# Kernel optimization log

Hardware: AMD Instinct MI355X
Metric: run time of the kernel (lower is better)

Reference implementation:

```python
import jax, jax.numpy as jnp
import numpy as np

B, S, HID = 1, 2048, 4096
N_HEADS, N_KV, HEAD_DIM = 32, 8, 128
N_REP = N_HEADS // N_KV
ROPE_THETA = 10000.0
NEG_INF = -1e9


def setup_inputs() -> dict:
    key = jax.random.key(0)
    ks = jax.random.split(key, 5)
    hidden_states = jax.random.normal(ks[0], (B, S, HID), dtype=jnp.float32)
    Wq = jax.random.normal(ks[1], (HID, N_HEADS * HEAD_DIM), dtype=jnp.float32) * 0.02
    Wk = jax.random.normal(ks[2], (HID, N_KV * HEAD_DIM), dtype=jnp.float32) * 0.02
    Wv = jax.random.normal(ks[3], (HID, N_KV * HEAD_DIM), dtype=jnp.float32) * 0.02
    Wo = jax.random.normal(ks[4], (N_HEADS * HEAD_DIM, HID), dtype=jnp.float32) * 0.02
    # causal additive mask [B, 1, S, S]
    causal = jnp.tril(jnp.ones((S, S), dtype=bool))
    attention_mask = jnp.where(causal, 0.0, NEG_INF).astype(jnp.float32)[None, None]
    position_ids = jnp.broadcast_to(jnp.arange(S, dtype=jnp.int32)[None], (B, S))
    return {
        "hidden_states": hidden_states, "Wq": Wq, "Wk": Wk, "Wv": Wv, "Wo": Wo,
        "attention_mask": attention_mask, "position_ids": position_ids,
    }


def _rotate_half(x):
    half = x.shape[-1] // 2
    return jnp.concatenate([-x[..., half:], x[..., :half]], axis=-1)


def _rope_tables(position_ids):
    # inv_freq: [head_dim/2]
    inv_freq = 1.0 / (ROPE_THETA ** (jnp.arange(0, HEAD_DIM, 2, dtype=jnp.float32) / HEAD_DIM))
    # freqs: [B, S, head_dim/2]
    freqs = position_ids.astype(jnp.float32)[..., None] * inv_freq
    emb = jnp.concatenate([freqs, freqs], axis=-1)  # [B, S, head_dim]
    # [B, 1, S, head_dim] to broadcast over heads
    return jnp.cos(emb)[:, None], jnp.sin(emb)[:, None]


def reference(hidden_states, Wq, Wk, Wv, Wo, attention_mask, position_ids):
    b, s, _ = hidden_states.shape
    # projections -> [B, H, S, D]
    q = (hidden_states @ Wq).reshape(b, s, N_HEADS, HEAD_DIM).transpose(0, 2, 1, 3)
    k = (hidden_states @ Wk).reshape(b, s, N_KV, HEAD_DIM).transpose(0, 2, 1, 3)
    v = (hidden_states @ Wv).reshape(b, s, N_KV, HEAD_DIM).transpose(0, 2, 1, 3)
    cos, sin = _rope_tables(position_ids)
    q = q * cos + _rotate_half(q) * sin
    k = k * cos + _rotate_half(k) * sin
    # GQA repeat_kv (repeat_interleave over head dim)
    k = jnp.repeat(k, N_REP, axis=1)
    v = jnp.repeat(v, N_REP, axis=1)
    scores = jnp.einsum("bhqd,bhkd->bhqk", q, k) / jnp.sqrt(jnp.float32(HEAD_DIM))
    scores = scores + attention_mask
    probs = jax.nn.softmax(scores.astype(jnp.float32), axis=-1).astype(q.dtype)
    attn = jnp.einsum("bhqk,bhkd->bhqd", probs, v)
    attn = attn.transpose(0, 2, 1, 3).reshape(b, s, N_HEADS * HEAD_DIM)
    return attn @ Wo
```

## Files before the change

### kernel.cpp

```cpp
#include <hip/hip_runtime.h>
#include <hip/hip_bf16.h>

#define S_LEN 2048
#define HIDDEN 4096
#define NH 32
#define NKV 8
#define HD 128
#define NQKV 6144

typedef __bf16 bf16_t;
typedef __bf16 bf16x8 __attribute__((ext_vector_type(8)));
typedef __bf16 bf16x4 __attribute__((ext_vector_type(4)));
typedef float f32x4 __attribute__((ext_vector_type(4)));

typedef __attribute__((address_space(1))) void gvoid;
typedef __attribute__((address_space(3))) void lvoid;

__device__ __forceinline__ void gload_lds16(const void* g, void* l) {
    __builtin_amdgcn_global_load_lds((gvoid*)g, (lvoid*)l, 16, 0, 0);
}

__device__ __forceinline__ float fast_exp2(float x) {
    return __builtin_amdgcn_exp2f(x);
}

__device__ __forceinline__ unsigned int pack2_bf16(float lo, float hi) {
    bf16_t l = (bf16_t)lo, h = (bf16_t)hi;
    unsigned short lu, hu;
    __builtin_memcpy(&lu, &l, 2);
    __builtin_memcpy(&hu, &h, 2);
    return ((unsigned int)hu << 16) | (unsigned int)lu;
}

__global__ __launch_bounds__(256) void prep_kernel(const float* __restrict__ hs,
                                                   const float* __restrict__ Wq,
                                                   const float* __restrict__ Wk,
                                                   const float* __restrict__ Wv,
                                                   const float* __restrict__ Wo,
                                                   bf16_t* __restrict__ hB,
                                                   bf16_t* __restrict__ WqkvT,
                                                   bf16_t* __restrict__ WoT) {
    __shared__ unsigned int t2[64][34];
    int b = blockIdx.x;
    const int t = threadIdx.x;
    if (b >= 10240) {
        int base = (b - 10240) * 1024 + t;
#pragma unroll
        for (int i = 0; i < 4; ++i) {
            int idx = base + i * 256;
            float4 v = ((const float4*)hs)[idx];
            bf16x4 o;
            o.x = (bf16_t)v.x; o.y = (bf16_t)v.y; o.z = (bf16_t)v.z; o.w = (bf16_t)v.w;
            ((bf16x4*)hB)[idx] = o;
        }
        return;
    }
    const float* in;
    bf16_t* out;
    int ldin, ldout, cx, ry;
    if (b < 4096) {
        in = Wq; out = WqkvT; ldin = HIDDEN; ldout = HIDDEN;
        cx = b & 63; ry = b >> 6;
    } else if (b < 5120) {
        b -= 4096;
        in = Wk; out = WqkvT + (size_t)4096 * HIDDEN; ldin = 1024; ldout = HIDDEN;
        cx = b & 15; ry = b >> 4;
    } else if (b < 6144) {
        b -= 5120;
        in = Wv; out = WqkvT + (size_t)5120 * HIDDEN; ldin = 1024; ldout = HIDDEN;
        cx = b & 15; ry = b >> 4;
    } else {
        b -= 6144;
        in = Wo; out = WoT; ldin = HIDDEN; ldout = HIDDEN;
        cx = b & 63; ry = b >> 6;
    }
    const int c0 = cx * 64, r0 = ry * 64;
    const int tx4 = t & 15, tp = t >> 4;
#pragma unroll
    for (int i = 0; i < 2; ++i) {
        int rp = tp + i * 16;
        const float* p0 = &in[(size_t)(r0 + 2 * rp) * ldin + c0 + tx4 * 4];
        float4 a = *(const float4*)p0;
        float4 bb = *(const float4*)(p0 + ldin);
        t2[tx4 * 4 + 0][rp] = pack2_bf16(a.x, bb.x);
        t2[tx4 * 4 + 1][rp] = pack2_bf16(a.y, bb.y);
        t2[tx4 * 4 + 2][rp] = pack2_bf16(a.z, bb.z);
        t2[tx4 * 4 + 3][rp] = pack2_bf16(a.w, bb.w);
    }
    __syncthreads();
    const int q = t & 3, cc = t >> 2;
    uint2 v0 = *(const uint2*)&t2[cc][q * 8 + 0];
    uint2 v1 = *(const uint2*)&t2[cc][q * 8 + 2];
    uint2 v2 = *(const uint2*)&t2[cc][q * 8 + 4];
    uint2 v3 = *(const uint2*)&t2[cc][q * 8 + 6];
    bf16_t* o = &out[(size_t)(c0 + cc) * ldout + r0 + q * 16];
    *(uint4*)o = make_uint4(v0.x, v0.y, v1.x, v1.y);
    *(uint4*)(o + 8) = make_uint4(v2.x, v2.y, v3.x, v3.y);
}

template<int BN, typename OutT>
__global__ __launch_bounds__(512, 2) void gemm_ring2_kernel(const bf16_t* __restrict__ A,
                                                            const bf16_t* __restrict__ Bt,
                                                            OutT* __restrict__ C,
                                                            int M, int N, int K) {
    constexpr int NF = BN / 32;
    __shared__ bf16_t As[3][256 * 32];
    __shared__ bf16_t Bs[3][BN * 32];
    const int tid = threadIdx.x;
    const int lane = tid & 63, w = tid >> 6;
    const int wm = w >> 1, wn = w & 1;
    const int g = lane >> 4, c16 = lane & 15;
    const int srow = lane >> 2;
    const int scg = ((lane & 3) ^ ((lane >> 3) & 3)) * 8;
    const int rdc = (g ^ ((c16 >> 1) & 3)) * 8;

    const int nbm = M / 256;
    const int cpx = gridDim.x >> 3;
    const int bid = blockIdx.x;
    const int swz = (bid & 7) * cpx + (bid >> 3);
    const int bm = swz % nbm, bn = swz / nbm;

    const bf16_t* Ab = A + (size_t)(bm * 256) * K;
    const bf16_t* Bb = Bt + (size_t)bn * BN * K;

    auto stage = [&](int slot, int kt) {
        const bf16_t* Ak = Ab + (size_t)kt * 32;
        const bf16_t* Bk = Bb + (size_t)kt * 32;
#pragma unroll
        for (int j = 0; j < 2; ++j) {
            int rb = 32 * w + 16 * j;
            gload_lds16(Ak + (size_t)(rb + srow) * K + scg, &As[slot][rb * 32]);
        }
        if constexpr (BN == 192) {
            if (w < 4) {
#pragma unroll
                for (int j = 0; j < 2; ++j) {
                    int rb = 32 * w + 16 * j;
                    gload_lds16(Bk + (size_t)(rb + srow) * K + scg, &Bs[slot][rb * 32]);
                }
            } else {
                int rb = 128 + 16 * (w - 4);
                gload_lds16(Bk + (size_t)(rb + srow) * K + scg, &Bs[slot][rb * 32]);
            }
        } else {
            int rb = 16 * w;
            gload_lds16(Bk + (size_t)(rb + srow) * K + scg, &Bs[slot][rb * 32]);
        }
    };

    f32x4 acc[4][NF];
#pragma unroll
    for (int i = 0; i < 4; ++i)
#pragma unroll
        for (int j = 0; j < NF; ++j)
            acc[i][j] = (f32x4){0.f, 0.f, 0.f, 0.f};

    const int NT = K / 32;
    stage(0, 0);
    stage(1, 1);

    int slot = 0, slot2 = 2;
    for (int t = 0; t < NT; ++t) {
        asm volatile("s_waitcnt vmcnt(3)" ::: "memory");
        __builtin_amdgcn_s_barrier();
        __builtin_amdgcn_sched_barrier(0);
        __builtin_amdgcn_s_setprio(1);

        bf16x8 af[4], bf[NF];
#pragma unroll
        for (int i = 0; i < 4; ++i) {
            int arow = wm * 64 + i * 16 + c16;
            af[i] = *(const bf16x8*)&As[slot][arow * 32 + rdc];
        }
#pragma unroll
        for (int j = 0; j < NF; ++j) {
            int brow = wn * (BN / 2) + j * 16 + c16;
            bf[j] = *(const bf16x8*)&Bs[slot][brow * 32 + rdc];
        }
        int nk = t + 2;
        if (nk >= NT) nk -= NT;
        stage(slot2, nk);

#pragma unroll
        for (int i = 0; i < 4; ++i)
#pragma unroll
            for (int j = 0; j < NF; ++j)
                acc[i][j] = __builtin_amdgcn_mfma_f32_16x16x32_bf16(af[i], bf[j], acc[i][j], 0, 0, 0);
        __builtin_amdgcn_s_setprio(0);

        slot = (slot + 1) % 3;
        slot2 = (slot2 + 1) % 3;
    }

#pragma unroll
    for (int mi = 0; mi < 4; ++mi)
#pragma unroll
        for (int ni = 0; ni < NF; ++ni) {
            int col = bn * BN + wn * (BN / 2) + ni * 16 + c16;
#pragma unroll
            for (int r = 0; r < 4; ++r) {
                int row = bm * 256 + wm * 64 + mi * 16 + g * 4 + r;
                C[(size_t)row * N + col] = (OutT)acc[mi][ni][r];
            }
        }
}

__global__ __launch_bounds__(256) void rope_vt_kernel(const bf16_t* __restrict__ qkv,
                                                      bf16_t* __restrict__ Qr,
                                                      bf16_t* __restrict__ Kr,
                                                      bf16_t* __restrict__ Vt,
                                                      const int* __restrict__ pos) {
    const int t = threadIdx.x;
    int b = blockIdx.x;
    if (b < 512) {
        __shared__ unsigned int t2[64][34];
        const int cx = b & 15, ry = b >> 4;
        const int c0 = cx * 64, r0 = ry * 64;
        const bf16_t* in = qkv + 5120;
        const int tx4 = t & 15, tp = t >> 4;
#pragma unroll
        for (int i = 0; i < 2; ++i) {
            int rp = tp + i * 16;
            const bf16_t* p0 = &in[(size_t)(r0 + 2 * rp) * NQKV + c0 + tx4 * 4];
            bf16x4 a = *(const bf16x4*)p0;
            bf16x4 bb = *(const bf16x4*)(p0 + NQKV);
#pragma unroll
            for (int k2 = 0; k2 < 4; ++k2) {
                unsigned short lu, hu;
                bf16_t la = a[k2], hb = bb[k2];
                __builtin_memcpy(&lu, &la, 2);
                __builtin_memcpy(&hu, &hb, 2);
                t2[tx4 * 4 + k2][rp] = ((unsigned int)hu << 16) | (unsigned int)lu;
            }
        }
        __syncthreads();
        const int q = t & 3, cc = t >> 2;
        uint2 v0 = *(const uint2*)&t2[cc][q * 8 + 0];
        uint2 v1 = *(const uint2*)&t2[cc][q * 8 + 2];
        uint2 v2 = *(const uint2*)&t2[cc][q * 8 + 4];
        uint2 v3 = *(const uint2*)&t2[cc][q * 8 + 6];
        bf16_t* o = &Vt[(size_t)(c0 + cc) * S_LEN + r0 + q * 16];
        *(uint4*)o = make_uint4(v0.x, v0.y, v1.x, v1.y);
        *(uint4*)(o + 8) = make_uint4(v2.x, v2.y, v3.x, v3.y);
        return;
    }
    int idx = (b - 512) * 256 + t;
    int total = S_LEN * 40 * 64;
    if (idx >= total) return;
    int d = idx & 63;
    int h = (idx >> 6) % 40;
    int s = idx / (64 * 40);
    int colbase = (h < 32) ? h * 128 : 4096 + (h - 32) * 128;
    bf16_t* ob = (h < 32) ? Qr + ((size_t)h * S_LEN + s) * HD
                          : Kr + ((size_t)(h - 32) * S_LEN + s) * HD;
    float scale = (h < 32) ? 0.1275174310f : 1.0f;
    const bf16_t* base = qkv + (size_t)s * NQKV + colbase;
    float x0 = (float)base[d], x1 = (float)base[d + 64];
    float p = (float)pos[s];
    float invf = fast_exp2(-0.20762050593046935f * (float)d);
    float f = p * invf;
    float sn, cs;
    __sincosf(f, &sn, &cs);
    float o0 = (x0 * cs - x1 * sn) * scale;
    float o1 = (x1 * cs + x0 * sn) * scale;
    ob[d] = (bf16_t)o0;
    ob[d + 64] = (bf16_t)o1;
}

#define PLD 68
__global__ __launch_bounds__(512) void attn_kernel(const bf16_t* __restrict__ Q,
                                                   const bf16_t* __restrict__ K,
                                                   const bf16_t* __restrict__ Vt,
                                                   bf16_t* __restrict__ O) {
    __shared__ bf16_t Ks[4][64 * 128];
    __shared__ bf16_t Vs[4][128 * 64];
    __shared__ bf16_t Pl[8][16 * PLD];
    const int tid = threadIdx.x;
    const int lane = tid & 63, w = tid >> 6;
    const int bid = blockIdx.x;
    const int h = bid & 31;
    const int x = bid >> 5;
    const int grp = w >> 2, wi = w & 3;
    const int kv = h >> 2;
    const int quad = lane >> 4, c16 = lane & 15;
    const int c7 = c16 & 7;
    const bf16_t* Qh = Q + (size_t)h * S_LEN * HD;
    const bf16_t* Kh = K + (size_t)kv * S_LEN * HD;
    const bf16_t* Vh = Vt + (size_t)kv * HD * S_LEN;
    bf16_t* P = Pl[w];

    auto stage = [&](int slot, int kb) {
        bf16_t* Kd = Ks[slot];
        bf16_t* Vd = Vs[slot];
#pragma unroll
        for (int j = 0; j < 2; ++j) {
            int i = w * 2 + j;
            {
                int row = 4 * i + (lane >> 4);
                int sc = (lane & 15) ^ (row & 7);
                gload_lds16(Kh + (size_t)(kb + row) * HD + sc * 8, Kd + i * 512);
            }
            {
                int row = 8 * i + (lane >> 3);
                int sc = (lane & 7) ^ ((lane >> 3) & 7);
                gload_lds16(Vh + (size_t)row * S_LEN + kb + sc * 8, Vd + i * 512);
            }
        }
    };

    bf16x8 ones;
#pragma unroll
    for (int j = 0; j < 8; ++j) ones[j] = (bf16_t)1.0f;

    for (int ph = 0; ph < 2; ++ph) {
        const int qt = (ph == 0) ? x : 15 - x;
        const int R = qt + 1;
        const int qb = qt * 128 + wi * 32;

        bf16x8 qf[2][4];
#pragma unroll
        for (int rg = 0; rg < 2; ++rg)
#pragma unroll
            for (int c = 0; c < 4; ++c)
                qf[rg][c] = *(const bf16x8*)(Qh + (size_t)(qb + rg * 16 + c16) * HD + c * 32 + quad * 8);

        f32x4 acc_o[2][8];
#pragma unroll
        for (int rg = 0; rg < 2; ++rg)
#pragma unroll
            for (int dt = 0; dt < 8; ++dt) acc_o[rg][dt] = (f32x4){0.f, 0.f, 0.f, 0.f};
        f32x4 acc_l[2] = {(f32x4){0.f, 0.f, 0.f, 0.f}, (f32x4){0.f, 0.f, 0.f, 0.f}};
        float m[2][4];
#pragma unroll
        for (int rg = 0; rg < 2; ++rg)
#pragma unroll
            for (int r = 0; r < 4; ++r) m[rg][r] = -1e30f;

        stage(0, 0);
        stage(1, 64);
        __syncthreads();

        for (int r = 0; r < R; ++r) {
            int jn0 = 2 * r + 2, jn1 = 2 * r + 3;
            if (jn0 < 2 * R) stage(jn0 & 3, jn0 * 64);
            if (jn1 < 2 * R) stage(jn1 & 3, jn1 * 64);

            const int j = 2 * r + grp;
            const int kb = j * 64;
            const bf16_t* Kb = Ks[j & 3];
            const bf16_t* Vb = Vs[j & 3];

            if (kb <= qb + 31) {
                const bool diag = (kb + 63 > qb);

                f32x4 sacc[2][4];
#pragma unroll
                for (int rg = 0; rg < 2; ++rg)
#pragma unroll
                    for (int t = 0; t < 4; ++t) sacc[rg][t] = (f32x4){0.f, 0.f, 0.f, 0.f};
#pragma unroll
                for (int t = 0; t < 4; ++t) {
                    const bf16_t* krow = Kb + (t * 16 + c16) * 128;
#pragma unroll
                    for (int cc = 0; cc < 4; ++cc) {
                        bf16x8 kf = *(const bf16x8*)(krow + (((cc * 4 + quad) ^ c7) * 8));
                        sacc[0][t] = __builtin_amdgcn_mfma_f32_16x16x32_bf16(qf[0][cc], kf, sacc[0][t], 0, 0, 0);
                        sacc[1][t] = __builtin_amdgcn_mfma_f32_16x16x32_bf16(qf[1][cc], kf, sacc[1][t], 0, 0, 0);
                    }
                }
                bf16x8 pf[2][2];
#pragma unroll
                for (int rg = 0; rg < 2; ++rg) {
                    float p[4][4], mxr[4];
#pragma unroll
                    for (int r4 = 0; r4 < 4; ++r4) {
                        int qq = qb + rg * 16 + quad * 4 + r4;
#pragma unroll
                        for (int t = 0; t < 4; ++t) {
                            float sv = sacc[rg][t][r4];
                            if (diag && (kb + t * 16 + c16 > qq)) sv = -1e30f;
                            p[t][r4] = sv;
                        }
                        float mx = fmaxf(fmaxf(p[0][r4], p[1][r4]), fmaxf(p[2][r4], p[3][r4]));
                        mx = fmaxf(mx, __shfl_xor(mx, 1));
                        mx = fmaxf(mx, __shfl_xor(mx, 2));
                        mx = fmaxf(mx, __shfl_xor(mx, 4));
                        mx = fmaxf(mx, __shfl_xor(mx, 8));
                        mxr[r4] = mx;
                    }
                    bool resc = false;
#pragma unroll
                    for (int r4 = 0; r4 < 4; ++r4) resc = resc || (mxr[r4] > m[rg][r4] + 8.f);
                    if (__any(resc)) {
#pragma unroll
                        for (int r4 = 0; r4 < 4; ++r4) {
                            float mn = fmaxf(m[rg][r4], mxr[r4]);
                            float al = fast_exp2(m[rg][r4] - mn);
                            m[rg][r4] = mn;
                            acc_l[rg][r4] *= al;
#pragma unroll
                            for (int dt = 0; dt < 8; ++dt) acc_o[rg][dt][r4] *= al;
                        }
                    }
#pragma unroll
                    for (int r4 = 0; r4 < 4; ++r4)
#pragma unroll
                        for (int t = 0; t < 4; ++t)
                            p[t][r4] = fast_exp2(p[t][r4] - m[rg][r4]);
#pragma unroll
                    for (int t = 0; t < 4; ++t)
#pragma unroll
                        for (int r4 = 0; r4 < 4; ++r4)
                            P[(quad * 4 + r4) * PLD + t * 16 + c16] = (bf16_t)p[t][r4];
                    pf[rg][0] = *(const bf16x8*)(P + c16 * PLD + quad * 8);
                    pf[rg][1] = *(const bf16x8*)(P + c16 * PLD + 32 + quad * 8);
                }
                acc_l[0] = __builtin_amdgcn_mfma_f32_16x16x32_bf16(pf[0][0], ones, acc_l[0], 0, 0, 0);
                acc_l[0] = __builtin_amdgcn_mfma_f32_16x16x32_bf16(pf[0][1], ones, acc_l[0], 0, 0, 0);
                acc_l[1] = __builtin_amdgcn_mfma_f32_16x16x32_bf16(pf[1][0], ones, acc_l[1], 0, 0, 0);
                acc_l[1] = __builtin_amdgcn_mfma_f32_16x16x32_bf16(pf[1][1], ones, acc_l[1], 0, 0, 0);
#pragma unroll
                for (int dt = 0; dt < 8; ++dt) {
                    const bf16_t* vrow = Vb + (dt * 16 + c16) * 64;
                    bf16x8 vf0 = *(const bf16x8*)(vrow + ((quad ^ c7) * 8));
                    bf16x8 vf1 = *(const bf16x8*)(vrow + (((4 + quad) ^ c7) * 8));
                    acc_o[0][dt] = __builtin_amdgcn_mfma_f32_16x16x32_bf16(pf[0][0], vf0, acc_o[0][dt], 0, 0, 0);
                    acc_o[0][dt] = __builtin_amdgcn_mfma_f32_16x16x32_bf16(pf[0][1], vf1, acc_o[0][dt], 0, 0, 0);
                    acc_o[1][dt] = __builtin_amdgcn_mfma_f32_16x16x32_bf16(pf[1][0], vf0, acc_o[1][dt], 0, 0, 0);
                    acc_o[1][dt] = __builtin_amdgcn_mfma_f32_16x16x32_bf16(pf[1][1], vf1, acc_o[1][dt], 0, 0, 0);
                }
            }
            __syncthreads();
        }

        float* s0 = (float*)&Ks[0][0];
        float* s1 = (float*)&Vs[0][0];
        const int sl = wi * 64 + lane;
        if (grp == 1) {
#pragma unroll
            for (int rg = 0; rg < 2; ++rg)
#pragma unroll
                for (int r4 = 0; r4 < 4; ++r4) {
                    s0[(rg * 4 + r4) * 256 + sl] = m[rg][r4];
                    s0[(8 + rg * 4 + r4) * 256 + sl] = acc_l[rg][r4];
                }
#pragma unroll
            for (int dt = 0; dt < 8; ++dt)
#pragma unroll
                for (int r4 = 0; r4 < 4; ++r4) {
                    s0[(16 + dt * 4 + r4) * 256 + sl] = acc_o[0][dt][r4];
                    s1[(dt * 4 + r4) * 256 + sl] = acc_o[1][dt][r4];
                }
        }
        __syncthreads();
        if (grp == 0) {
#pragma unroll
            for (int rg = 0; rg < 2; ++rg)
#pragma unroll
                for (int r4 = 0; r4 < 4; ++r4) {
                    float m1 = s0[(rg * 4 + r4) * 256 + sl];
                    float l1 = s0[(8 + rg * 4 + r4) * 256 + sl];
                    float mm = fmaxf(m[rg][r4], m1);
                    float a0 = fast_exp2(m[rg][r4] - mm);
                    float a1 = fast_exp2(m1 - mm);
                    float ll = acc_l[rg][r4] * a0 + l1 * a1;
                    float inv = 1.f / ll;
                    bf16_t* orow = &O[(size_t)(qb + rg * 16 + quad * 4 + r4) * HIDDEN + h * HD];
#pragma unroll
                    for (int dt = 0; dt < 8; ++dt) {
                        float o1 = (rg == 0) ? s0[(16 + dt * 4 + r4) * 256 + sl]
                                             : s1[(dt * 4 + r4) * 256 + sl];
                        float val = (acc_o[rg][dt][r4] * a0 + o1 * a1) * inv;
                        orow[dt * 16 + c16] = (bf16_t)val;
                    }
                }
        }
        __syncthreads();
    }
}

extern "C" void kernel_launch(void* const* d_in, const int* in_sizes, int n_in,
                              void* d_out, int out_size, void* d_ws, size_t ws_size,
                              hipStream_t stream) {
    const float* hs = (const float*)d_in[0];
    const float* Wq = (const float*)d_in[1];
    const float* Wk = (const float*)d_in[2];
    const float* Wv = (const float*)d_in[3];
    const float* Wo = (const float*)d_in[4];
    const int* pos = (const int*)d_in[6];
    float* out = (float*)d_out;

    char* ws = (char*)d_ws;
    size_t off = 0;
    auto alloc = [&](size_t bytes) -> void* {
        void* p = ws + off;
        off += (bytes + 255) & ~(size_t)255;
        return p;
    };
    bf16_t* hB    = (bf16_t*)alloc((size_t)S_LEN * HIDDEN * 2);
    bf16_t* WqkvT = (bf16_t*)alloc((size_t)NQKV * HIDDEN * 2);
    bf16_t* WoT   = (bf16_t*)alloc((size_t)HIDDEN * HIDDEN * 2);
    bf16_t* QKV   = (bf16_t*)alloc((size_t)S_LEN * NQKV * 2);
    bf16_t* Qr    = (bf16_t*)alloc((size_t)NH * S_LEN * HD * 2);
    bf16_t* Kr    = (bf16_t*)alloc((size_t)NKV * S_LEN * HD * 2);
    bf16_t* Vt    = (bf16_t*)alloc((size_t)NKV * HD * S_LEN * 2);
    bf16_t* Oat   = (bf16_t*)alloc((size_t)S_LEN * HIDDEN * 2);

    prep_kernel<<<12288, 256, 0, stream>>>(hs, Wq, Wk, Wv, Wo, hB, WqkvT, WoT);
    gemm_ring2_kernel<192, bf16_t><<<(S_LEN / 256) * (NQKV / 192), 512, 0, stream>>>(hB, WqkvT, QKV, S_LEN, NQKV, HIDDEN);
    rope_vt_kernel<<<512 + (S_LEN * 40 * 64 + 255) / 256, 256, 0, stream>>>(QKV, Qr, Kr, Vt, pos);
    attn_kernel<<<256, 512, 0, stream>>>(Qr, Kr, Vt, Oat);
    gemm_ring2_kernel<128, float><<<(S_LEN / 256) * (HIDDEN / 128), 512, 0, stream>>>(Oat, WoT, out, S_LEN, HIDDEN, HIDDEN);
}
```

Baseline: 316.2 us.

## Add 256x256 ping-pong GEMM kernel with quarter-tile staging for QKV projection

Adds a new GEMM kernel that computes a 256x256 output tile per 512-thread block, split into four 128x128 quadrants. The A and B halves are double-buffered in LDS and loaded asynchronously in quarter steps interleaved with the MFMA work, using priority bumps and barriers between steps. The QKV projection now uses this kernel instead of the 256x192 ring-buffer GEMM. The goal is better operand reuse and more overlap of loads with compute. In exchange the kernel runs one large block per CU with heavy register use, the grid shrinks to 192 blocks, and the fp32 accumulators are written to C with scalar, uncoalesced stores.

```diff
diff --git a/kernel.cpp b/kernel.cpp
--- a/kernel.cpp
+++ b/kernel.cpp
@@ -96,6 +96,153 @@
     bf16_t* o = &out[(size_t)(c0 + cc) * ldout + r0 + q * 16];
     *(uint4*)o = make_uint4(v0.x, v0.y, v1.x, v1.y);
     *(uint4*)(o + 8) = make_uint4(v2.x, v2.y, v3.x, v3.y);
+}
+
+template<typename OutT>
+__global__ __launch_bounds__(512) void gemm_deep_kernel(const bf16_t* __restrict__ A,
+                                                        const bf16_t* __restrict__ Bt,
+                                                        OutT* __restrict__ C,
+                                                        int M, int N, int K) {
+    __shared__ bf16_t As[2][2][128 * 64];
+    __shared__ bf16_t Bs[2][2][128 * 64];
+    __shared__ bf16_t Sc[128 * 64];
+    const int tid = threadIdx.x;
+    const int lane = tid & 63, w = tid >> 6;
+    const int wm = w >> 2, wn = w & 3;
+    const int g = lane >> 4, c16 = lane & 15;
+    const int c7 = c16 & 7;
+
+    const int nbm = M / 256;
+    const int cpx = gridDim.x >> 3;
+    const int swz = (blockIdx.x & 7) * cpx + (blockIdx.x >> 3);
+    const int bm = swz % nbm, bn = swz / nbm;
+
+    const bf16_t* Abase = A + (size_t)(bm * 256) * K;
+    const bf16_t* Bbase = Bt + (size_t)(bn * 256) * K;
+    const int NT = K / 64;
+
+    auto stageHalf = [&](int cur) {
+        int tile = cur >> 2, type = cur & 3;
+        bool dummy = (tile >= NT);
+        int kt = dummy ? 0 : tile;
+        int par = tile & 1;
+        int h = type >> 1;
+        if ((type & 1) == 0) {
+            bf16_t* dst = dummy ? Sc : As[par][h];
+#pragma unroll
+            for (int j = 0; j < 2; ++j) {
+                int idx = j * 512 + tid;
+                int r = idx >> 3;
+                int grow = (r & 63) + ((r >> 6) << 7) + h * 64;
+                int gcol = kt * 64 + (((idx & 7) ^ (r & 7)) << 3);
+                gload_lds16(Abase + (size_t)grow * K + gcol, dst + (size_t)(j * 512 + (w << 6)) * 8);
+            }
+        } else {
+            bf16_t* dst = dummy ? Sc : Bs[par][h];
+#pragma unroll
+            for (int j = 0; j < 2; ++j) {
+                int idx = j * 512 + tid;
+                int r = idx >> 3;
+                int grow = ((r >> 5) << 6) + h * 32 + (r & 31);
+                int gcol = kt * 64 + (((idx & 7) ^ (r & 7)) << 3);
+                gload_lds16(Bbase + (size_t)grow * K + gcol, dst + (size_t)(j * 512 + (w << 6)) * 8);
+            }
+        }
+    };
+    auto rdA = [&](int par, int h, bf16x8 (&a)[2][4]) {
+        const bf16_t* base = &As[par][h][0];
+#pragma unroll
+        for (int kk = 0; kk < 2; ++kk)
+#pragma unroll
+            for (int mi = 0; mi < 4; ++mi) {
+                int r = wm * 64 + mi * 16 + c16;
+                a[kk][mi] = *(const bf16x8*)&base[r * 64 + (((kk * 4 + g) ^ c7) << 3)];
+            }
+    };
+    auto rdB = [&](int par, int h, bf16x8 (&b)[2][2]) {
+        const bf16_t* base = &Bs[par][h][0];
+#pragma unroll
+        for (int kk = 0; kk < 2; ++kk)
+#pragma unroll
+            for (int nn = 0; nn < 2; ++nn) {
+                int r = wn * 32 + nn * 16 + c16;
+                b[kk][nn] = *(const bf16x8*)&base[r * 64 + (((kk * 4 + g) ^ c7) << 3)];
+            }
+    };
+
+    f32x4 acc00[4][2], acc10[4][2], acc11[4][2], acc01[4][2];
+#pragma unroll
+    for (int mi = 0; mi < 4; ++mi)
+#pragma unroll
+        for (int nn = 0; nn < 2; ++nn) {
+            acc00[mi][nn] = (f32x4){0.f, 0.f, 0.f, 0.f};
+            acc10[mi][nn] = (f32x4){0.f, 0.f, 0.f, 0.f};
+            acc11[mi][nn] = (f32x4){0.f, 0.f, 0.f, 0.f};
+            acc01[mi][nn] = (f32x4){0.f, 0.f, 0.f, 0.f};
+        }
+    auto MM = [&](bf16x8 (&a)[2][4], bf16x8 (&b)[2][2], f32x4 (&acc)[4][2]) {
+#pragma unroll
+        for (int kk = 0; kk < 2; ++kk)
+#pragma unroll
+            for (int mi = 0; mi < 4; ++mi)
+#pragma unroll
+                for (int nn = 0; nn < 2; ++nn)
+                    acc[mi][nn] = __builtin_amdgcn_mfma_f32_16x16x32_bf16(a[kk][mi], b[kk][nn], acc[mi][nn], 0, 0, 0);
+    };
+
+    for (int c = 0; c < 7; ++c) stageHalf(c);
+    asm volatile("s_waitcnt vmcnt(6)" ::: "memory");
+    __builtin_amdgcn_s_barrier();
+    __builtin_amdgcn_sched_barrier(0);
+
+    int cur = 7;
+    bf16x8 a0[2][4], a1[2][4], b0[2][2], b1[2][2];
+    for (int t = 0; t < NT; ++t) {
+        const int par = t & 1;
+        __builtin_amdgcn_s_setprio(1);
+        rdA(par, 0, a0); rdB(par, 0, b0);
+        stageHalf(cur++);
+        MM(a0, b0, acc00);
+        __builtin_amdgcn_s_setprio(0);
+        __builtin_amdgcn_s_barrier();
+        __builtin_amdgcn_sched_barrier(0);
+        __builtin_amdgcn_s_setprio(1);
+        rdA(par, 1, a1);
+        stageHalf(cur++);
+        MM(a1, b0, acc10);
+        __builtin_amdgcn_s_setprio(0);
+        __builtin_amdgcn_s_barrier();
+        __builtin_amdgcn_sched_barrier(0);
+        __builtin_amdgcn_s_setprio(1);
+        rdB(par, 1, b1);
+        stageHalf(cur++);
+        MM(a1, b1, acc11);
+        __builtin_amdgcn_s_setprio(0);
+        __builtin_amdgcn_s_barrier();
+        __builtin_amdgcn_sched_barrier(0);
+        asm volatile("s_waitcnt vmcnt(4)" ::: "memory");
+        __builtin_amdgcn_s_setprio(1);
+        stageHalf(cur++);
+        MM(a0, b1, acc01);
+        __builtin_amdgcn_s_setprio(0);
+        __builtin_amdgcn_s_barrier();
+        __builtin_amdgcn_sched_barrier(0);
+    }
+
+    auto wr = [&](f32x4 (&acc)[4][2], int mh, int nh) {
+#pragma unroll
+        for (int mi = 0; mi < 4; ++mi)
+#pragma unroll
+            for (int nn = 0; nn < 2; ++nn) {
+                int col = bn * 256 + wn * 64 + nh * 32 + nn * 16 + c16;
+#pragma unroll
+                for (int r = 0; r < 4; ++r) {
+                    int row = bm * 256 + wm * 128 + mh * 64 + mi * 16 + g * 4 + r;
+                    C[(size_t)row * N + col] = (OutT)acc[mi][nn][r];
+                }
+            }
+    };
+    wr(acc00, 0, 0); wr(acc10, 1, 0); wr(acc11, 1, 1); wr(acc01, 0, 1);
 }
 
 template<int BN, typename OutT>
@@ -507,7 +654,7 @@
     bf16_t* Oat   = (bf16_t*)alloc((size_t)S_LEN * HIDDEN * 2);
 
     prep_kernel<<<12288, 256, 0, stream>>>(hs, Wq, Wk, Wv, Wo, hB, WqkvT, WoT);
-    gemm_ring2_kernel<192, bf16_t><<<(S_LEN / 256) * (NQKV / 192), 512, 0, stream>>>(hB, WqkvT, QKV, S_LEN, NQKV, HIDDEN);
+    gemm_deep_kernel<bf16_t><<<(S_LEN / 256) * (NQKV / 256), 512, 0, stream>>>(hB, WqkvT, QKV, S_LEN, NQKV, HIDDEN);
     rope_vt_kernel<<<512 + (S_LEN * 40 * 64 + 255) / 256, 256, 0, stream>>>(QKV, Qr, Kr, Vt, pos);
     attn_kernel<<<256, 512, 0, stream>>>(Qr, Kr, Vt, Oat);
     gemm_ring2_kernel<128, float><<<(S_LEN / 256) * (HIDDEN / 128), 512, 0, stream>>>(Oat, WoT, out, S_LEN, HIDDEN, HIDDEN);
```

Result: no change. 316.8 us (+0.2%).
